# Kernel optimization log

Hardware: AMD Instinct MI355X
Metric: run time of the kernel (lower is better)

The kernel has to match this reference:

```python
import jax, jax.numpy as jnp
import numpy as np

B, N, S, K = 8, 4096, 1024, 16
C_IN, C_OUT = 128, 256
BN_EPS = 1e-5


def setup_inputs() -> dict:
    key = jax.random.key(0)
    ks = jax.random.split(key, 20)
    sc = 0.02
    p = {
        'xyz': jax.random.normal(ks[0], (B, N, 3), jnp.float32),
        'points': jax.random.normal(ks[1], (B, N, C_IN), jnp.float32),
        'wq': jax.random.normal(ks[2], (C_IN, C_OUT), jnp.float32) * sc,
        'wk': jax.random.normal(ks[3], (C_IN, C_OUT), jnp.float32) * sc,
        'wv': jax.random.normal(ks[4], (C_IN, C_OUT), jnp.float32) * sc,
        'dw1': jax.random.normal(ks[5], (3, C_OUT), jnp.float32) * sc,
        'db1': jnp.zeros((C_OUT,), jnp.float32),
        'dw2': jax.random.normal(ks[6], (C_OUT, C_OUT), jnp.float32) * sc,
        'db2': jnp.zeros((C_OUT,), jnp.float32),
        'gw1': jax.random.normal(ks[7], (C_OUT, C_OUT), jnp.float32) * sc,
        'gb1': jnp.zeros((C_OUT,), jnp.float32),
        'gw2': jax.random.normal(ks[8], (C_OUT, C_OUT), jnp.float32) * sc,
        'gb2': jnp.zeros((C_OUT,), jnp.float32),
        'lw': jax.random.normal(ks[9], (C_OUT, C_OUT), jnp.float32) * sc,
        'lb': jnp.zeros((C_OUT,), jnp.float32),
        'bn_g': jnp.ones((C_OUT,), jnp.float32),
        'bn_b': jnp.zeros((C_OUT,), jnp.float32),
    }
    return p


def _fps(xyz, npoint):
    # xyz: [N,3] -> farthest point sample indices [npoint] (deterministic start at 0,
    # matching torch impl with fixed seed semantics)
    n = xyz.shape[0]
    def step(carry, _):
        dist, far = carry
        centroid = xyz[far]                      # [3]
        d = jnp.sum((xyz - centroid) ** 2, -1)   # [N]
        dist = jnp.minimum(dist, d)
        return (dist, jnp.argmax(dist).astype(jnp.int32)), far
    init = (jnp.full((n,), 1e10, xyz.dtype), jnp.int32(0))
    _, idx = jax.lax.scan(step, init, None, length=npoint)
    return idx  # [npoint]


def _mlp2(x, w1, b1, w2, b2):
    return jax.nn.relu(x @ w1 + b1) @ w2 + b2


def reference(xyz, points, wq, wk, wv, dw1, db1, dw2, db2,
              gw1, gb1, gw2, gb2, lw, lb, bn_g, bn_b):
    # --- sample_and_group (FPS + KNN, knn=True) ---
    fps_idx = jax.vmap(lambda x: _fps(x, S))(xyz)                 # [B,S]
    new_xyz = jnp.take_along_axis(xyz, fps_idx[..., None], 1)     # [B,S,3]
    # squared distances sampled->all: [B,S,N]
    d2 = (jnp.sum(new_xyz**2, -1)[:, :, None]
          - 2.0 * jnp.einsum('bsc,bnc->bsn', new_xyz, xyz)
          + jnp.sum(xyz**2, -1)[:, None, :])
    knn_idx = jax.lax.top_k(-d2, K)[1]                            # [B,S,K]
    gather = jax.vmap(lambda a, i: a[i])
    knn_xyz = gather(xyz, knn_idx)                                # [B,S,K,3]
    knn_xyz_norm = knn_xyz - new_xyz[:, :, None]                  # centered coords
    knn_points = gather(points, knn_idx)                          # [B,S,K,C_in]
    sampled_points = jnp.take_along_axis(points, fps_idx[..., None], 1)  # [B,S,C_in]

    # --- vector attention ---
    q = sampled_points @ wq                                       # [B,S,C_out]
    k = knn_points @ wk                                           # [B,S,K,C_out]
    v = knn_points @ wv                                           # [B,S,K,C_out]
    pos_enc = _mlp2(knn_xyz_norm, dw1, db1, dw2, db2)             # [B,S,K,C_out]
    att = _mlp2(q[:, :, None] - k + pos_enc, gw1, gb1, gw2, gb2)  # [B,S,K,C_out]
    att = jax.nn.softmax(att / np.sqrt(C_OUT).astype(np.float32), axis=-2)
    res = jnp.einsum('bmnf,bmnf->bmf', att, v + pos_enc)          # [B,S,C_out]

    # --- fc_last + BatchNorm1d (training-mode batch stats, biased var) + ReLU ---
    res = res @ lw + lb
    mean = jnp.mean(res, axis=(0, 1))
    var = jnp.var(res, axis=(0, 1))
    res = bn_g * (res - mean) * jax.lax.rsqrt(var + BN_EPS) + bn_b
    res = jax.nn.relu(res)
    return new_xyz, res
```

## Files before the change

### kernel.cpp

```cpp
#include <hip/hip_runtime.h>

typedef unsigned long long ull;
typedef __attribute__((ext_vector_type(8))) short bf16x8;
typedef __attribute__((ext_vector_type(4))) float f32x4;

__device__ __forceinline__ unsigned short bf16b(float x){
    unsigned u = __float_as_uint(x);
    unsigned r = (u + 0x7FFFu + ((u >> 16) & 1u)) >> 16;
    return (unsigned short)r;
}
__device__ __forceinline__ float b2f(unsigned short u){
    return __uint_as_float(((unsigned)u) << 16);
}
__device__ __forceinline__ void st4(unsigned short* p, f32x4 v){
    ull pk = (ull)bf16b(v[0]) | (((ull)bf16b(v[1])) << 16)
           | (((ull)bf16b(v[2])) << 32) | (((ull)bf16b(v[3])) << 48);
    *(ull*)p = pk;
}
__device__ __forceinline__ f32x4 ld4(const unsigned short* p){
    ull pk = *(const ull*)p;
    f32x4 v;
    v[0] = b2f((unsigned short)pk);
    v[1] = b2f((unsigned short)(pk >> 16));
    v[2] = b2f((unsigned short)(pk >> 32));
    v[3] = b2f((unsigned short)(pk >> 48));
    return v;
}

#define DPPMAX(k, ctrl) do { \
    unsigned _lo = (unsigned)(k), _hi = (unsigned)((k) >> 32); \
    unsigned _l2 = (unsigned)__builtin_amdgcn_update_dpp((int)_lo, (int)_lo, (ctrl), 0xF, 0xF, false); \
    unsigned _h2 = (unsigned)__builtin_amdgcn_update_dpp((int)_hi, (int)_hi, (ctrl), 0xF, 0xF, false); \
    ull _k2 = (((ull)_h2) << 32) | _l2; \
    if (_k2 > (k)) (k) = _k2; \
} while (0)
#define DPPMIN(k, ctrl) do { \
    unsigned _lo = (unsigned)(k), _hi = (unsigned)((k) >> 32); \
    unsigned _l2 = (unsigned)__builtin_amdgcn_update_dpp((int)_lo, (int)_lo, (ctrl), 0xF, 0xF, false); \
    unsigned _h2 = (unsigned)__builtin_amdgcn_update_dpp((int)_hi, (int)_hi, (ctrl), 0xF, 0xF, false); \
    ull _k2 = (((ull)_h2) << 32) | _l2; \
    if (_k2 < (k)) (k) = _k2; \
} while (0)

template<int KT>
__device__ __forceinline__ int swz(int r, int c){
    return r * (KT * 32) + ((((c >> 3) + r) & (KT * 4 - 1)) << 3) + (c & 7);
}

template<int KT>
__device__ __forceinline__ void gemmT(const unsigned short* __restrict__ Wt,
                                      const unsigned short* __restrict__ Blds,
                                      int ch0, int lane, f32x4 acc[4][4])
{
    int i = lane & 15, q = lane >> 4;
#pragma unroll
    for (int kt = 0; kt < KT; kt++){
        int k0 = kt * 32 + q * 8;
        bf16x8 bfr[4], afr[4];
#pragma unroll
        for (int nt = 0; nt < 4; nt++)
            bfr[nt] = *(const bf16x8*)(Blds + swz<KT>(nt * 16 + i, k0));
#pragma unroll
        for (int mt = 0; mt < 4; mt++)
            afr[mt] = *(const bf16x8*)(Wt + (size_t)(ch0 + mt * 16 + i) * (KT * 32) + k0);
#pragma unroll
        for (int mt = 0; mt < 4; mt++)
#pragma unroll
            for (int nt = 0; nt < 4; nt++)
                acc[mt][nt] = __builtin_amdgcn_mfma_f32_16x16x32_bf16(afr[mt], bfr[nt], acc[mt][nt], 0, 0, 0);
    }
}

#define ZERO44(A) do { _Pragma("unroll") for (int _m = 0; _m < 4; _m++) \
    { _Pragma("unroll") for (int _n = 0; _n < 4; _n++) { A[_m][_n][0]=0.f;A[_m][_n][1]=0.f;A[_m][_n][2]=0.f;A[_m][_n][3]=0.f; } } } while(0)

__global__ __launch_bounds__(512, 2) void fps_mega(
    const float* __restrict__ xyz, float* __restrict__ nxyz_out, int* __restrict__ fps_idx,
    const float* __restrict__ pts, unsigned short* __restrict__ pts16,
    const float* __restrict__ wq, const float* __restrict__ wk, const float* __restrict__ wv,
    const float* __restrict__ dw2, const float* __restrict__ gw1, const float* __restrict__ gw2,
    const float* __restrict__ lw,
    float* __restrict__ wqT, unsigned short* __restrict__ wkT, unsigned short* __restrict__ wvT,
    unsigned short* __restrict__ dw2T, unsigned short* __restrict__ gw1T,
    unsigned short* __restrict__ gw2T, unsigned short* __restrict__ lwT,
    float* __restrict__ stats)
{
    __shared__ float sx[4096], sy[4096], sz[4096];
    __shared__ int farS[1024];
    __shared__ ull slotK[2][8];

    int blk = blockIdx.x;
    int t = threadIdx.x;

    if (blk >= 8){
        int aux = blk - 8;
        if (aux < 704){
            if (aux == 0) stats[t] = 0.f;
            int i = aux * 512 + t;
            if (i < 32768){ int n = i >> 7, k = i & 127; wqT[i] = wq[k * 256 + n]; return; } i -= 32768;
            if (i < 32768){ int n = i >> 7, k = i & 127; wkT[i] = bf16b(wk[k * 256 + n]); return; } i -= 32768;
            if (i < 32768){ int n = i >> 7, k = i & 127; wvT[i] = bf16b(wv[k * 256 + n]); return; } i -= 32768;
            if (i < 65536){ int n = i >> 8, k = i & 255; dw2T[i] = bf16b(dw2[k * 256 + n]); return; } i -= 65536;
            if (i < 65536){ int n = i >> 8, k = i & 255; gw1T[i] = bf16b(gw1[k * 256 + n]); return; } i -= 65536;
            if (i < 65536){ int n = i >> 8, k = i & 255; gw2T[i] = bf16b(gw2[k * 256 + n]); return; } i -= 65536;
            if (i < 65536){ int n = i >> 8, k = i & 255; lwT[i]  = bf16b(lw[k * 256 + n]); return; }
            return;
        }
        int i = ((aux - 704) * 512 + t) * 4;
        f32x4 v = *(const f32x4*)(pts + i);
        ull pk = (ull)bf16b(v[0]) | (((ull)bf16b(v[1])) << 16)
               | (((ull)bf16b(v[2])) << 32) | (((ull)bf16b(v[3])) << 48);
        *(ull*)(pts16 + i) = pk;
        return;
    }

    int b = blk;
    int lane = t & 63, wvi = t >> 6;
    for (int p = t; p < 4096; p += 512){
        const float* s = xyz + ((size_t)b * 4096 + p) * 3;
        sx[p] = s[0]; sy[p] = s[1]; sz[p] = s[2];
    }
    __syncthreads();
    float px[8], py[8], pz[8], dist[8];
    unsigned nplo[8];
#pragma unroll
    for (int j = 0; j < 8; j++){
        int p = t + (j << 9);
        px[j] = sx[p]; py[j] = sy[p]; pz[j] = sz[p];
        dist[j] = 1e10f;
        nplo[j] = ~(unsigned)p;
        asm volatile("" : "+v"(px[j]), "+v"(py[j]), "+v"(pz[j]), "+v"(nplo[j]));
    }
    int far = 0;
    float cx = sx[0], cy = sy[0], cz = sz[0];
    int par = 0;
    for (int s = 0; s < 1024; s++){
        if (t == 0) farS[s] = far;
        ull lb = 0;
#pragma unroll
        for (int j = 0; j < 8; j++){
            float dx = __fsub_rn(px[j], cx);
            float dy = __fsub_rn(py[j], cy);
            float dz = __fsub_rn(pz[j], cz);
            float d = __fadd_rn(__fadd_rn(__fmul_rn(dx, dx), __fmul_rn(dy, dy)), __fmul_rn(dz, dz));
            float nd = fminf(dist[j], d);
            dist[j] = nd;
            ull k2 = (((ull)__float_as_uint(nd)) << 32) | nplo[j];
            if (k2 > lb) lb = k2;
        }
        DPPMAX(lb, 0xB1); DPPMAX(lb, 0x4E); DPPMAX(lb, 0x141);
        DPPMAX(lb, 0x140); DPPMAX(lb, 0x142); DPPMAX(lb, 0x143);
        if (lane == 63) slotK[par][wvi] = lb;
        __syncthreads();
        ull k = slotK[par][lane & 7];
        DPPMAX(k, 0xB1); DPPMAX(k, 0x4E); DPPMAX(k, 0x141);
        far = (int)(~(unsigned)k);
        cx = sx[far]; cy = sy[far]; cz = sz[far];
        par ^= 1;
    }
    float* outp = nxyz_out + (size_t)b * 3072;
    for (int s2 = t; s2 < 1024; s2 += 512){
        int f = farS[s2];
        fps_idx[b * 1024 + s2] = f;
        outp[s2 * 3 + 0] = sx[f];
        outp[s2 * 3 + 1] = sy[f];
        outp[s2 * 3 + 2] = sz[f];
    }
}

__global__ __launch_bounds__(256) void knn_kernel(const float* __restrict__ xyz,
                                                  const float* __restrict__ nxyz,
                                                  int* __restrict__ knn_idx)
{
    __shared__ float d2s[4096];
    __shared__ ull kslot[4];
    int G = blockIdx.x; int b = G >> 10;
    int t = threadIdx.x, lane = t & 63, wvi = t >> 6;
    float qx = nxyz[(size_t)G * 3], qy = nxyz[(size_t)G * 3 + 1], qz = nxyz[(size_t)G * 3 + 2];
    float qq = qx * qx + qy * qy + qz * qz;
    for (int j = 0; j < 16; j++){
        int p = t + (j << 8);
        const float* s = xyz + ((size_t)b * 4096 + p) * 3;
        float x = s[0], y = s[1], z = s[2];
        d2s[p] = qq - 2.f * (qx * x + qy * y + qz * z) + (x * x + y * y + z * z);
    }
    __syncthreads();
    for (int r = 0; r < 16; r++){
        ull best = ~0ull;
#pragma unroll
        for (int j = 0; j < 16; j++){
            int p = t + (j << 8);
            unsigned bb = __float_as_uint(d2s[p]);
            bb = (bb & 0x80000000u) ? ~bb : (bb | 0x80000000u);
            ull key = (((ull)bb) << 32) | (unsigned)p;
            if (key < best) best = key;
        }
        DPPMIN(best, 0xB1); DPPMIN(best, 0x4E); DPPMIN(best, 0x141);
        DPPMIN(best, 0x140); DPPMIN(best, 0x142); DPPMIN(best, 0x143);
        if (lane == 63) kslot[wvi] = best;
        __syncthreads();
        if (t == 0){
            ull bk = kslot[0];
            for (int w = 1; w < 4; w++) if (kslot[w] < bk) bk = kslot[w];
            int p = (int)(unsigned)bk;
            knn_idx[(size_t)G * 16 + r] = p;
            d2s[p] = 3.0e38f;
        }
        __syncthreads();
    }
}

__global__ __launch_bounds__(256) void q_kernel(const float* __restrict__ points,
                                                const float* __restrict__ wqT,
                                                const int* __restrict__ fps_idx,
                                                float* __restrict__ qbuf)
{
    __shared__ float sp[8][128];
    int t = threadIdx.x;
    int g0 = blockIdx.x * 8;
    {
        int r = t >> 5, c = (t & 31) * 4;
        int G = g0 + r; int b = G >> 10; int p = fps_idx[G];
        const f32x4 v = *(const f32x4*)(points + ((size_t)b * 4096 + p) * 128 + c);
        *(f32x4*)&sp[r][c] = v;
    }
    __syncthreads();
    float acc[8] = {0.f,0.f,0.f,0.f,0.f,0.f,0.f,0.f};
    const float* wr = wqT + t * 128;
    for (int k = 0; k < 128; k += 4){
        f32x4 w = *(const f32x4*)(wr + k);
#pragma unroll
        for (int r = 0; r < 8; r++)
            acc[r] += w[0]*sp[r][k] + w[1]*sp[r][k+1] + w[2]*sp[r][k+2] + w[3]*sp[r][k+3];
    }
#pragma unroll
    for (int r = 0; r < 8; r++) qbuf[(size_t)(g0 + r) * 256 + t] = acc[r];
}

__global__ __launch_bounds__(256, 2) void fused_attn(
    const unsigned short* __restrict__ pts16,
    const float* __restrict__ xyz, const float* __restrict__ nxyz,
    const int* __restrict__ knn_idx, const float* __restrict__ qbuf,
    const unsigned short* __restrict__ wkT, const unsigned short* __restrict__ wvT,
    const unsigned short* __restrict__ dw2T, const unsigned short* __restrict__ gw1T,
    const unsigned short* __restrict__ gw2T,
    const float* __restrict__ dw1, const float* __restrict__ db1,
    const float* __restrict__ db2, const float* __restrict__ gb1, const float* __restrict__ gb2,
    unsigned short* __restrict__ resY)
{
    __shared__ unsigned short bufA[16384];
    __shared__ unsigned short bufU[16384];
    int t = threadIdx.x, lane = t & 63, wave = t >> 6;
    int i = lane & 15, q = lane >> 4;
    int G0 = blockIdx.x * 4;
    int ch0 = wave * 64;
    unsigned short* ptsA = bufU;
    float* dw1s  = (float*)(bufU + 8192);
    float* db1s  = (float*)(bufU + 9728);
    float* xyznS = (float*)(bufU + 10240);
    int*   idxs  = (int*)  (bufU + 10624);

    if (t < 64) idxs[t] = knn_idx[G0 * 16 + t];
    dw1s[t] = dw1[t]; dw1s[256 + t] = dw1[256 + t]; dw1s[512 + t] = dw1[512 + t];
    db1s[t] = db1[t];
    __syncthreads();

    if (t < 64){
        int G = G0 + (t >> 4); int bb = G >> 10; int p = idxs[t];
        const float* xp = xyz + ((size_t)bb * 4096 + p) * 3;
        const float* nz = nxyz + (size_t)G * 3;
        xyznS[t * 3 + 0] = xp[0] - nz[0];
        xyznS[t * 3 + 1] = xp[1] - nz[1];
        xyznS[t * 3 + 2] = xp[2] - nz[2];
    }
    {
        int r = t >> 2, seg = t & 3;
        int G = G0 + (r >> 4); int bb = G >> 10; int p = idxs[r];
        const uint4* src = (const uint4*)(pts16 + ((size_t)bb * 4096 + p) * 128 + seg * 32);
#pragma unroll
        for (int j = 0; j < 4; j++){
            uint4 v = src[j];
            *(uint4*)(ptsA + swz<4>(r, seg * 32 + j * 8)) = v;
        }
    }
    __syncthreads();

    {
        int r = lane;
        int o0 = wave * 64;
        float x = xyznS[r * 3], y = xyznS[r * 3 + 1], z = xyznS[r * 3 + 2];
#pragma unroll
        for (int j = 0; j < 64; j += 4){
            int o = o0 + j;
            f32x4 v;
#pragma unroll
            for (int e = 0; e < 4; e++)
                v[e] = fmaxf(db1s[o + e] + x * dw1s[o + e] + y * dw1s[256 + o + e] + z * dw1s[512 + o + e], 0.f);
            st4(bufA + swz<8>(r, o), v);
        }
    }
    __syncthreads();

    f32x4 accP[4][4]; ZERO44(accP);
    gemmT<8>(dw2T, bufA, ch0, lane, accP);
#pragma unroll
    for (int mt = 0; mt < 4; mt++){
        f32x4 d2v = *(const f32x4*)(db2 + ch0 + mt * 16 + q * 4);
#pragma unroll
        for (int nt = 0; nt < 4; nt++) accP[mt][nt] += d2v;
    }
    f32x4 accK[4][4]; ZERO44(accK);
    gemmT<4>(wkT, ptsA, ch0, lane, accK);
    __syncthreads();

#pragma unroll
    for (int mt = 0; mt < 4; mt++){
        int c = ch0 + mt * 16 + q * 4;
#pragma unroll
        for (int nt = 0; nt < 4; nt++){
            int r = nt * 16 + i;
            f32x4 qv = *(const f32x4*)(qbuf + (size_t)(G0 + nt) * 256 + c);
            f32x4 tv = qv - accK[mt][nt] + accP[mt][nt];
            st4(bufA + swz<8>(r, c), tv);
        }
    }
    f32x4 accV[4][4]; ZERO44(accV);
    gemmT<4>(wvT, ptsA, ch0, lane, accV);
    __syncthreads();

#pragma unroll
    for (int mt = 0; mt < 4; mt++){
        int c = ch0 + mt * 16 + q * 4;
#pragma unroll
        for (int nt = 0; nt < 4; nt++){
            int r = nt * 16 + i;
            f32x4 uv = accV[mt][nt] + accP[mt][nt];
            st4(bufU + swz<8>(r, c), uv);
        }
    }
    f32x4 acc1[4][4]; ZERO44(acc1);
    gemmT<8>(gw1T, bufA, ch0, lane, acc1);
    __syncthreads();

#pragma unroll
    for (int mt = 0; mt < 4; mt++){
        int c = ch0 + mt * 16 + q * 4;
        f32x4 g1v = *(const f32x4*)(gb1 + c);
#pragma unroll
        for (int nt = 0; nt < 4; nt++){
            int r = nt * 16 + i;
            f32x4 av = acc1[mt][nt] + g1v;
#pragma unroll
            for (int e = 0; e < 4; e++) av[e] = fmaxf(av[e], 0.f);
            st4(bufA + swz<8>(r, c), av);
        }
    }
    __syncthreads();

    f32x4 acc2[4][4]; ZERO44(acc2);
    gemmT<8>(gw2T, bufA, ch0, lane, acc2);
    __syncthreads();

#pragma unroll
    for (int mt = 0; mt < 4; mt++){
        int c = ch0 + mt * 16 + q * 4;
        f32x4 g2v = *(const f32x4*)(gb2 + c);
#pragma unroll
        for (int nt = 0; nt < 4; nt++){
            int r = nt * 16 + i;
            f32x4 ev;
#pragma unroll
            for (int e = 0; e < 4; e++) ev[e] = __expf((acc2[mt][nt][e] + g2v[e]) * 0.0625f);
            st4(bufA + swz<8>(r, c), ev);
        }
    }
    __syncthreads();

    {
        int g = t >> 6, c4 = (t & 63) * 4;
        f32x4 num; num[0]=0.f;num[1]=0.f;num[2]=0.f;num[3]=0.f;
        f32x4 den = num;
#pragma unroll
        for (int rr = 0; rr < 16; rr++){
            int r = g * 16 + rr;
            f32x4 e4 = ld4(bufA + swz<8>(r, c4));
            f32x4 u4 = ld4(bufU + swz<8>(r, c4));
            num += e4 * u4;
            den += e4;
        }
        f32x4 rv = num / den;
        st4(resY + (size_t)(G0 + g) * 256 + c4, rv);
    }
}

__global__ __launch_bounds__(256, 2) void z_gemm(const unsigned short* __restrict__ resY,
                                                 const unsigned short* __restrict__ lwT,
                                                 const float* __restrict__ lb,
                                                 float* __restrict__ zbuf,
                                                 float* __restrict__ stats)
{
    int t = threadIdx.x, lane = t & 63, wave = t >> 6;
    int i = lane & 15, q = lane >> 4;
    int row0 = blockIdx.x * 128;
    int ch0 = wave * 64;
    f32x4 acc[4][8];
#pragma unroll
    for (int mt = 0; mt < 4; mt++)
#pragma unroll
        for (int nt = 0; nt < 8; nt++){ acc[mt][nt][0]=0.f;acc[mt][nt][1]=0.f;acc[mt][nt][2]=0.f;acc[mt][nt][3]=0.f; }
#pragma unroll
    for (int kt = 0; kt < 8; kt++){
        int k0 = kt * 32 + q * 8;
        bf16x8 a[4], bb[8];
#pragma unroll
        for (int mt = 0; mt < 4; mt++)
            a[mt] = *(const bf16x8*)(lwT + (size_t)(ch0 + mt * 16 + i) * 256 + k0);
#pragma unroll
        for (int nt = 0; nt < 8; nt++)
            bb[nt] = *(const bf16x8*)(resY + (size_t)(row0 + nt * 16 + i) * 256 + k0);
#pragma unroll
        for (int mt = 0; mt < 4; mt++)
#pragma unroll
            for (int nt = 0; nt < 8; nt++)
                acc[mt][nt] = __builtin_amdgcn_mfma_f32_16x16x32_bf16(a[mt], bb[nt], acc[mt][nt], 0, 0, 0);
    }
    f32x4 s1[4], s2[4];
#pragma unroll
    for (int mt = 0; mt < 4; mt++){ s1[mt][0]=0.f;s1[mt][1]=0.f;s1[mt][2]=0.f;s1[mt][3]=0.f; s2[mt]=s1[mt]; }
#pragma unroll
    for (int mt = 0; mt < 4; mt++){
        int c = ch0 + mt * 16 + q * 4;
        f32x4 lb4 = *(const f32x4*)(lb + c);
#pragma unroll
        for (int nt = 0; nt < 8; nt++){
            int r = row0 + nt * 16 + i;
            f32x4 z = acc[mt][nt] + lb4;
            *(f32x4*)(zbuf + (size_t)r * 256 + c) = z;
            s1[mt] += z;
            s2[mt] += z * z;
        }
    }
    for (int m = 1; m < 16; m <<= 1){
#pragma unroll
        for (int mt = 0; mt < 4; mt++)
#pragma unroll
            for (int e = 0; e < 4; e++){
                s1[mt][e] += __shfl_xor(s1[mt][e], m);
                s2[mt][e] += __shfl_xor(s2[mt][e], m);
            }
    }
    if (i == 0){
#pragma unroll
        for (int mt = 0; mt < 4; mt++){
            int c = ch0 + mt * 16 + q * 4;
#pragma unroll
            for (int e = 0; e < 4; e++){
                atomicAdd(&stats[c + e], s1[mt][e]);
                atomicAdd(&stats[256 + c + e], s2[mt][e]);
            }
        }
    }
}

__global__ __launch_bounds__(256) void bn_kernel(const float* __restrict__ zbuf,
                                                 const float* __restrict__ stats,
                                                 const float* __restrict__ bn_g,
                                                 const float* __restrict__ bn_b,
                                                 float* __restrict__ out)
{
    int G = blockIdx.x, c = threadIdx.x;
    float mean = stats[c] * (1.f / 8192.f);
    float var = stats[256 + c] * (1.f / 8192.f) - mean * mean;
    float inv = rsqrtf(var + 1e-5f);
    float z = zbuf[(size_t)G * 256 + c];
    float y = bn_g[c] * (z - mean) * inv + bn_b[c];
    out[24576 + (size_t)G * 256 + c] = fmaxf(y, 0.f);
}

extern "C" void kernel_launch(void* const* d_in, const int* in_sizes, int n_in,
                              void* d_out, int out_size, void* d_ws, size_t ws_size,
                              hipStream_t stream)
{
    const float* xyz    = (const float*)d_in[0];
    const float* points = (const float*)d_in[1];
    const float* wq  = (const float*)d_in[2];
    const float* wk  = (const float*)d_in[3];
    const float* wv  = (const float*)d_in[4];
    const float* dw1 = (const float*)d_in[5];
    const float* db1 = (const float*)d_in[6];
    const float* dw2 = (const float*)d_in[7];
    const float* db2 = (const float*)d_in[8];
    const float* gw1 = (const float*)d_in[9];
    const float* gb1 = (const float*)d_in[10];
    const float* gw2 = (const float*)d_in[11];
    const float* gb2 = (const float*)d_in[12];
    const float* lw  = (const float*)d_in[13];
    const float* lb  = (const float*)d_in[14];
    const float* bn_g = (const float*)d_in[15];
    const float* bn_b = (const float*)d_in[16];
    float* out = (float*)d_out;

    char* ws = (char*)d_ws;
    int*            fps_idx = (int*)(ws + 0);
    int*            knn_idx = (int*)(ws + 32768);
    float*          qbuf    = (float*)(ws + 557056);
    unsigned short* pts16   = (unsigned short*)(ws + 8945664);
    unsigned short* wkT     = (unsigned short*)(ws + 17334272);
    unsigned short* wvT     = (unsigned short*)(ws + 17399808);
    unsigned short* dw2T    = (unsigned short*)(ws + 17465344);
    unsigned short* gw1T    = (unsigned short*)(ws + 17596416);
    unsigned short* gw2T    = (unsigned short*)(ws + 17727488);
    unsigned short* lwT     = (unsigned short*)(ws + 17858560);
    float*          wqT     = (float*)(ws + 17989632);
    unsigned short* resY    = (unsigned short*)(ws + 18120704);
    float*          zbuf    = (float*)(ws + 22315008);
    float*          stats   = (float*)(ws + 30703616);

    fps_mega<<<2760, 512, 0, stream>>>(xyz, out, fps_idx, points, pts16,
                                       wq, wk, wv, dw2, gw1, gw2, lw,
                                       wqT, wkT, wvT, dw2T, gw1T, gw2T, lwT, stats);
    knn_kernel<<<8192, 256, 0, stream>>>(xyz, out, knn_idx);
    q_kernel<<<1024, 256, 0, stream>>>(points, wqT, fps_idx, qbuf);
    fused_attn<<<2048, 256, 0, stream>>>(pts16, xyz, out, knn_idx, qbuf,
                                         wkT, wvT, dw2T, gw1T, gw2T,
                                         dw1, db1, db2, gb1, gb2, resY);
    z_gemm<<<64, 256, 0, stream>>>(resY, lwT, lb, zbuf, stats);
    bn_kernel<<<8192, 256, 0, stream>>>(zbuf, stats, bn_g, bn_b, out);
}
```

Measured before the change: 1.051 ms.

## Use packed FP32 math and split float-max/index reduction in FPS loop

The farthest-point-sampling inner loop now computes squared distances with packed v_pk_add/v_pk_mul on pairs of points. The per-wave argmax is split into two steps: a 32-bit float max reduction across the wave, then a second 32-bit DPP reduction over the indices whose distance equals that max. This replaces the 64-bit key reduction, which needed two DPP moves and a 64-bit compare per step. Index tie-breaking is kept by selecting the largest inverted index. Rounding differs slightly because the subtraction is done as an add of the negated centroid, though this should give the same result.

```diff
diff --git a/kernel.cpp b/kernel.cpp
--- a/kernel.cpp
+++ b/kernel.cpp
@@ -3,6 +3,7 @@
 typedef unsigned long long ull;
 typedef __attribute__((ext_vector_type(8))) short bf16x8;
 typedef __attribute__((ext_vector_type(4))) float f32x4;
+typedef __attribute__((ext_vector_type(2))) float f32x2;
 
 __device__ __forceinline__ unsigned short bf16b(float x){
     unsigned u = __float_as_uint(x);
@@ -25,6 +26,13 @@
     v[2] = b2f((unsigned short)(pk >> 32));
     v[3] = b2f((unsigned short)(pk >> 48));
     return v;
+}
+
+__device__ __forceinline__ f32x2 pk_add(f32x2 a, f32x2 b){
+    f32x2 r; asm("v_pk_add_f32 %0, %1, %2" : "=v"(r) : "v"(a), "v"(b)); return r;
+}
+__device__ __forceinline__ f32x2 pk_mul(f32x2 a, f32x2 b){
+    f32x2 r; asm("v_pk_mul_f32 %0, %1, %2" : "=v"(r) : "v"(a), "v"(b)); return r;
 }
 
 #define DPPMAX(k, ctrl) do { \
@@ -41,6 +49,15 @@
     ull _k2 = (((ull)_h2) << 32) | _l2; \
     if (_k2 < (k)) (k) = _k2; \
 } while (0)
+#define DPPMAXF(x, ctrl) do { \
+    float _o = __uint_as_float((unsigned)__builtin_amdgcn_update_dpp( \
+        (int)__float_as_uint(x), (int)__float_as_uint(x), (ctrl), 0xF, 0xF, false)); \
+    (x) = fmaxf((x), _o); \
+} while (0)
+#define DPPMAXU(x, ctrl) do { \
+    unsigned _o = (unsigned)__builtin_amdgcn_update_dpp((int)(x), (int)(x), (ctrl), 0xF, 0xF, false); \
+    (x) = (_o > (x)) ? _o : (x); \
+} while (0)
 
 template<int KT>
 __device__ __forceinline__ int swz(int r, int c){
@@ -121,36 +138,61 @@
         sx[p] = s[0]; sy[p] = s[1]; sz[p] = s[2];
     }
     __syncthreads();
-    float px[8], py[8], pz[8], dist[8];
+    f32x2 px2[4], py2[4], pz2[4];
+    float dist[8];
     unsigned nplo[8];
 #pragma unroll
-    for (int j = 0; j < 8; j++){
-        int p = t + (j << 9);
-        px[j] = sx[p]; py[j] = sy[p]; pz[j] = sz[p];
-        dist[j] = 1e10f;
-        nplo[j] = ~(unsigned)p;
-        asm volatile("" : "+v"(px[j]), "+v"(py[j]), "+v"(pz[j]), "+v"(nplo[j]));
+    for (int k = 0; k < 4; k++){
+        int p0 = t + (k << 10), p1 = p0 + 512;
+        px2[k][0] = sx[p0]; px2[k][1] = sx[p1];
+        py2[k][0] = sy[p0]; py2[k][1] = sy[p1];
+        pz2[k][0] = sz[p0]; pz2[k][1] = sz[p1];
+        dist[2*k] = 1e10f; dist[2*k+1] = 1e10f;
+        nplo[2*k] = ~(unsigned)p0; nplo[2*k+1] = ~(unsigned)p1;
+        asm volatile("" : "+v"(px2[k]), "+v"(py2[k]), "+v"(pz2[k]));
     }
     int far = 0;
     float cx = sx[0], cy = sy[0], cz = sz[0];
     int par = 0;
     for (int s = 0; s < 1024; s++){
         if (t == 0) farS[s] = far;
-        ull lb = 0;
-#pragma unroll
-        for (int j = 0; j < 8; j++){
-            float dx = __fsub_rn(px[j], cx);
-            float dy = __fsub_rn(py[j], cy);
-            float dz = __fsub_rn(pz[j], cz);
-            float d = __fadd_rn(__fadd_rn(__fmul_rn(dx, dx), __fmul_rn(dy, dy)), __fmul_rn(dz, dz));
-            float nd = fminf(dist[j], d);
-            dist[j] = nd;
-            ull k2 = (((ull)__float_as_uint(nd)) << 32) | nplo[j];
-            if (k2 > lb) lb = k2;
-        }
-        DPPMAX(lb, 0xB1); DPPMAX(lb, 0x4E); DPPMAX(lb, 0x141);
-        DPPMAX(lb, 0x140); DPPMAX(lb, 0x142); DPPMAX(lb, 0x143);
-        if (lane == 63) slotK[par][wvi] = lb;
+        f32x2 ncx, ncy, ncz;
+        ncx[0] = -cx; ncx[1] = -cx;
+        ncy[0] = -cy; ncy[1] = -cy;
+        ncz[0] = -cz; ncz[1] = -cz;
+        float bmax = 0.f;
+#pragma unroll
+        for (int k = 0; k < 4; k++){
+            f32x2 dx = pk_add(px2[k], ncx);
+            f32x2 dy = pk_add(py2[k], ncy);
+            f32x2 dz = pk_add(pz2[k], ncz);
+            f32x2 d2 = pk_add(pk_add(pk_mul(dx, dx), pk_mul(dy, dy)), pk_mul(dz, dz));
+            float n0 = fminf(dist[2*k],     d2[0]);
+            float n1 = fminf(dist[2*k + 1], d2[1]);
+            dist[2*k] = n0; dist[2*k+1] = n1;
+            bmax = fmaxf(bmax, fmaxf(n0, n1));
+        }
+        DPPMAXF(bmax, 0xB1); DPPMAXF(bmax, 0x4E); DPPMAXF(bmax, 0x141);
+        DPPMAXF(bmax, 0x140); DPPMAXF(bmax, 0x142); DPPMAXF(bmax, 0x143);
+        unsigned wmb = (unsigned)__builtin_amdgcn_readlane((int)__float_as_uint(bmax), 63);
+        unsigned c0 = (__float_as_uint(dist[0]) == wmb) ? nplo[0] : 0u;
+        unsigned c1 = (__float_as_uint(dist[1]) == wmb) ? nplo[1] : 0u;
+        unsigned c2 = (__float_as_uint(dist[2]) == wmb) ? nplo[2] : 0u;
+        unsigned c3 = (__float_as_uint(dist[3]) == wmb) ? nplo[3] : 0u;
+        unsigned c4 = (__float_as_uint(dist[4]) == wmb) ? nplo[4] : 0u;
+        unsigned c5 = (__float_as_uint(dist[5]) == wmb) ? nplo[5] : 0u;
+        unsigned c6 = (__float_as_uint(dist[6]) == wmb) ? nplo[6] : 0u;
+        unsigned c7 = (__float_as_uint(dist[7]) == wmb) ? nplo[7] : 0u;
+        unsigned m0 = c0 > c1 ? c0 : c1;
+        unsigned m1 = c2 > c3 ? c2 : c3;
+        unsigned m2 = c4 > c5 ? c4 : c5;
+        unsigned m3 = c6 > c7 ? c6 : c7;
+        m0 = m0 > m1 ? m0 : m1;
+        m2 = m2 > m3 ? m2 : m3;
+        unsigned cand = m0 > m2 ? m0 : m2;
+        DPPMAXU(cand, 0xB1); DPPMAXU(cand, 0x4E); DPPMAXU(cand, 0x141);
+        DPPMAXU(cand, 0x140); DPPMAXU(cand, 0x142); DPPMAXU(cand, 0x143);
+        if (lane == 63) slotK[par][wvi] = (((ull)wmb) << 32) | (ull)cand;
         __syncthreads();
         ull k = slotK[par][lane & 7];
         DPPMAX(k, 0xB1); DPPMAX(k, 0x4E); DPPMAX(k, 0x141);
```

New measurement: 1.111 ms. 5.6% more time.

## Fuse FPS, KNN, query and attention into persistent kernel overlapping FPS progress

Applied to the files above, without the earlier changes.

Replaces the separate FPS, KNN, q-projection and attention kernels with one persistent 256-block kernel. Eight blocks run FPS and publish progress every 16 samples through atomic counters. The other blocks first do the weight and points preprocessing, then spin-wait and process 8-centroid chunks (KNN, q, attention) as soon as their centroids are ready. This hides the serial FPS latency behind the downstream work, at the cost of spin-wait synchronisation and a reliance on all 256 blocks being co-resident. ctrl aliases the zbuf region, which is only written later by z_gemm.

```diff
diff --git a/kernel.cpp b/kernel.cpp
--- a/kernel.cpp
+++ b/kernel.cpp
@@ -74,112 +74,16 @@
 #define ZERO44(A) do { _Pragma("unroll") for (int _m = 0; _m < 4; _m++) \
     { _Pragma("unroll") for (int _n = 0; _n < 4; _n++) { A[_m][_n][0]=0.f;A[_m][_n][1]=0.f;A[_m][_n][2]=0.f;A[_m][_n][3]=0.f; } } } while(0)
 
-__global__ __launch_bounds__(512, 2) void fps_mega(
-    const float* __restrict__ xyz, float* __restrict__ nxyz_out, int* __restrict__ fps_idx,
-    const float* __restrict__ pts, unsigned short* __restrict__ pts16,
-    const float* __restrict__ wq, const float* __restrict__ wk, const float* __restrict__ wv,
-    const float* __restrict__ dw2, const float* __restrict__ gw1, const float* __restrict__ gw2,
-    const float* __restrict__ lw,
-    float* __restrict__ wqT, unsigned short* __restrict__ wkT, unsigned short* __restrict__ wvT,
-    unsigned short* __restrict__ dw2T, unsigned short* __restrict__ gw1T,
-    unsigned short* __restrict__ gw2T, unsigned short* __restrict__ lwT,
-    float* __restrict__ stats)
-{
-    __shared__ float sx[4096], sy[4096], sz[4096];
-    __shared__ int farS[1024];
-    __shared__ ull slotK[2][8];
-
-    int blk = blockIdx.x;
-    int t = threadIdx.x;
-
-    if (blk >= 8){
-        int aux = blk - 8;
-        if (aux < 704){
-            if (aux == 0) stats[t] = 0.f;
-            int i = aux * 512 + t;
-            if (i < 32768){ int n = i >> 7, k = i & 127; wqT[i] = wq[k * 256 + n]; return; } i -= 32768;
-            if (i < 32768){ int n = i >> 7, k = i & 127; wkT[i] = bf16b(wk[k * 256 + n]); return; } i -= 32768;
-            if (i < 32768){ int n = i >> 7, k = i & 127; wvT[i] = bf16b(wv[k * 256 + n]); return; } i -= 32768;
-            if (i < 65536){ int n = i >> 8, k = i & 255; dw2T[i] = bf16b(dw2[k * 256 + n]); return; } i -= 65536;
-            if (i < 65536){ int n = i >> 8, k = i & 255; gw1T[i] = bf16b(gw1[k * 256 + n]); return; } i -= 65536;
-            if (i < 65536){ int n = i >> 8, k = i & 255; gw2T[i] = bf16b(gw2[k * 256 + n]); return; } i -= 65536;
-            if (i < 65536){ int n = i >> 8, k = i & 255; lwT[i]  = bf16b(lw[k * 256 + n]); return; }
-            return;
-        }
-        int i = ((aux - 704) * 512 + t) * 4;
-        f32x4 v = *(const f32x4*)(pts + i);
-        ull pk = (ull)bf16b(v[0]) | (((ull)bf16b(v[1])) << 16)
-               | (((ull)bf16b(v[2])) << 32) | (((ull)bf16b(v[3])) << 48);
-        *(ull*)(pts16 + i) = pk;
-        return;
-    }
-
-    int b = blk;
-    int lane = t & 63, wvi = t >> 6;
-    for (int p = t; p < 4096; p += 512){
-        const float* s = xyz + ((size_t)b * 4096 + p) * 3;
-        sx[p] = s[0]; sy[p] = s[1]; sz[p] = s[2];
-    }
-    __syncthreads();
-    float px[8], py[8], pz[8], dist[8];
-    unsigned nplo[8];
-#pragma unroll
-    for (int j = 0; j < 8; j++){
-        int p = t + (j << 9);
-        px[j] = sx[p]; py[j] = sy[p]; pz[j] = sz[p];
-        dist[j] = 1e10f;
-        nplo[j] = ~(unsigned)p;
-        asm volatile("" : "+v"(px[j]), "+v"(py[j]), "+v"(pz[j]), "+v"(nplo[j]));
-    }
-    int far = 0;
-    float cx = sx[0], cy = sy[0], cz = sz[0];
-    int par = 0;
-    for (int s = 0; s < 1024; s++){
-        if (t == 0) farS[s] = far;
-        ull lb = 0;
-#pragma unroll
-        for (int j = 0; j < 8; j++){
-            float dx = __fsub_rn(px[j], cx);
-            float dy = __fsub_rn(py[j], cy);
-            float dz = __fsub_rn(pz[j], cz);
-            float d = __fadd_rn(__fadd_rn(__fmul_rn(dx, dx), __fmul_rn(dy, dy)), __fmul_rn(dz, dz));
-            float nd = fminf(dist[j], d);
-            dist[j] = nd;
-            ull k2 = (((ull)__float_as_uint(nd)) << 32) | nplo[j];
-            if (k2 > lb) lb = k2;
-        }
-        DPPMAX(lb, 0xB1); DPPMAX(lb, 0x4E); DPPMAX(lb, 0x141);
-        DPPMAX(lb, 0x140); DPPMAX(lb, 0x142); DPPMAX(lb, 0x143);
-        if (lane == 63) slotK[par][wvi] = lb;
-        __syncthreads();
-        ull k = slotK[par][lane & 7];
-        DPPMAX(k, 0xB1); DPPMAX(k, 0x4E); DPPMAX(k, 0x141);
-        far = (int)(~(unsigned)k);
-        cx = sx[far]; cy = sy[far]; cz = sz[far];
-        par ^= 1;
-    }
-    float* outp = nxyz_out + (size_t)b * 3072;
-    for (int s2 = t; s2 < 1024; s2 += 512){
-        int f = farS[s2];
-        fps_idx[b * 1024 + s2] = f;
-        outp[s2 * 3 + 0] = sx[f];
-        outp[s2 * 3 + 1] = sy[f];
-        outp[s2 * 3 + 2] = sz[f];
-    }
-}
-
-__global__ __launch_bounds__(256) void knn_kernel(const float* __restrict__ xyz,
-                                                  const float* __restrict__ nxyz,
-                                                  int* __restrict__ knn_idx)
-{
-    __shared__ float d2s[4096];
-    __shared__ ull kslot[4];
-    int G = blockIdx.x; int b = G >> 10;
-    int t = threadIdx.x, lane = t & 63, wvi = t >> 6;
+__device__ __forceinline__ void knn_one(int t2, int G,
+        const float* __restrict__ xyz, const float* __restrict__ nxyz,
+        int* __restrict__ knn_idx, float* d2s, ull* kslot)
+{
+    int b = G >> 10;
+    int lane = t2 & 63, wvi = t2 >> 6;
     float qx = nxyz[(size_t)G * 3], qy = nxyz[(size_t)G * 3 + 1], qz = nxyz[(size_t)G * 3 + 2];
     float qq = qx * qx + qy * qy + qz * qz;
     for (int j = 0; j < 16; j++){
-        int p = t + (j << 8);
+        int p = t2 + (j << 8);
         const float* s = xyz + ((size_t)b * 4096 + p) * 3;
         float x = s[0], y = s[1], z = s[2];
         d2s[p] = qq - 2.f * (qx * x + qy * y + qz * z) + (x * x + y * y + z * z);
@@ -189,7 +93,7 @@
         ull best = ~0ull;
 #pragma unroll
         for (int j = 0; j < 16; j++){
-            int p = t + (j << 8);
+            int p = t2 + (j << 8);
             unsigned bb = __float_as_uint(d2s[p]);
             bb = (bb & 0x80000000u) ? ~bb : (bb | 0x80000000u);
             ull key = (((ull)bb) << 32) | (unsigned)p;
@@ -199,7 +103,7 @@
         DPPMIN(best, 0x140); DPPMIN(best, 0x142); DPPMIN(best, 0x143);
         if (lane == 63) kslot[wvi] = best;
         __syncthreads();
-        if (t == 0){
+        if (t2 == 0){
             ull bk = kslot[0];
             for (int w = 1; w < 4; w++) if (kslot[w] < bk) bk = kslot[w];
             int p = (int)(unsigned)bk;
@@ -210,34 +114,7 @@
     }
 }
 
-__global__ __launch_bounds__(256) void q_kernel(const float* __restrict__ points,
-                                                const float* __restrict__ wqT,
-                                                const int* __restrict__ fps_idx,
-                                                float* __restrict__ qbuf)
-{
-    __shared__ float sp[8][128];
-    int t = threadIdx.x;
-    int g0 = blockIdx.x * 8;
-    {
-        int r = t >> 5, c = (t & 31) * 4;
-        int G = g0 + r; int b = G >> 10; int p = fps_idx[G];
-        const f32x4 v = *(const f32x4*)(points + ((size_t)b * 4096 + p) * 128 + c);
-        *(f32x4*)&sp[r][c] = v;
-    }
-    __syncthreads();
-    float acc[8] = {0.f,0.f,0.f,0.f,0.f,0.f,0.f,0.f};
-    const float* wr = wqT + t * 128;
-    for (int k = 0; k < 128; k += 4){
-        f32x4 w = *(const f32x4*)(wr + k);
-#pragma unroll
-        for (int r = 0; r < 8; r++)
-            acc[r] += w[0]*sp[r][k] + w[1]*sp[r][k+1] + w[2]*sp[r][k+2] + w[3]*sp[r][k+3];
-    }
-#pragma unroll
-    for (int r = 0; r < 8; r++) qbuf[(size_t)(g0 + r) * 256 + t] = acc[r];
-}
-
-__global__ __launch_bounds__(256, 2) void fused_attn(
+__device__ void attn_unit(int t, char* base, int G0,
     const unsigned short* __restrict__ pts16,
     const float* __restrict__ xyz, const float* __restrict__ nxyz,
     const int* __restrict__ knn_idx, const float* __restrict__ qbuf,
@@ -248,11 +125,10 @@
     const float* __restrict__ db2, const float* __restrict__ gb1, const float* __restrict__ gb2,
     unsigned short* __restrict__ resY)
 {
-    __shared__ unsigned short bufA[16384];
-    __shared__ unsigned short bufU[16384];
-    int t = threadIdx.x, lane = t & 63, wave = t >> 6;
+    unsigned short* bufA = (unsigned short*)base;
+    unsigned short* bufU = (unsigned short*)(base + 32768);
+    int lane = t & 63, wave = t >> 6;
     int i = lane & 15, q = lane >> 4;
-    int G0 = blockIdx.x * 4;
     int ch0 = wave * 64;
     unsigned short* ptsA = bufU;
     float* dw1s  = (float*)(bufU + 8192);
@@ -390,6 +266,187 @@
         }
         f32x4 rv = num / den;
         st4(resY + (size_t)(G0 + g) * 256 + c4, rv);
+    }
+}
+
+__device__ void do_chunk(int t, int c, char* SM,
+    const float* __restrict__ xyz, const float* __restrict__ nxyz,
+    const float* __restrict__ points, const float* __restrict__ wqT,
+    const int* __restrict__ fps_idx, int* __restrict__ knn_idx, float* __restrict__ qbuf,
+    const unsigned short* __restrict__ pts16,
+    const unsigned short* __restrict__ wkT, const unsigned short* __restrict__ wvT,
+    const unsigned short* __restrict__ dw2T, const unsigned short* __restrict__ gw1T,
+    const unsigned short* __restrict__ gw2T,
+    const float* __restrict__ dw1, const float* __restrict__ db1,
+    const float* __restrict__ db2, const float* __restrict__ gb1, const float* __restrict__ gb2,
+    unsigned short* __restrict__ resY)
+{
+    int g0 = c * 8;
+    int sub = t >> 8, t2 = t & 255;
+    float* d2s = (float*)(SM + sub * 16384);
+    ull* kslot = (ull*)(SM + 131072) + sub * 4;
+    for (int r4 = 0; r4 < 4; r4++)
+        knn_one(t2, g0 + r4 * 2 + sub, xyz, nxyz, knn_idx, d2s, kslot);
+    __syncthreads();
+    {
+        float* sp = (float*)SM;
+        if (t < 256){
+            int r = t >> 5, c4 = (t & 31) * 4;
+            int G = g0 + r; int b = G >> 10; int p = fps_idx[G];
+            *(f32x4*)(sp + r * 128 + c4) = *(const f32x4*)(points + ((size_t)b * 4096 + p) * 128 + c4);
+        }
+        __syncthreads();
+        float acc[4] = {0.f, 0.f, 0.f, 0.f};
+        const float* wr = wqT + t2 * 128;
+        for (int k = 0; k < 128; k += 4){
+            f32x4 w = *(const f32x4*)(wr + k);
+#pragma unroll
+            for (int r = 0; r < 4; r++){
+                const float* row = sp + (sub * 4 + r) * 128;
+                acc[r] += w[0]*row[k] + w[1]*row[k+1] + w[2]*row[k+2] + w[3]*row[k+3];
+            }
+        }
+#pragma unroll
+        for (int r = 0; r < 4; r++) qbuf[(size_t)(g0 + sub * 4 + r) * 256 + t2] = acc[r];
+        __syncthreads();
+    }
+    attn_unit(t2, SM + sub * 65536, g0 + sub * 4, pts16, xyz, nxyz, knn_idx, qbuf,
+              wkT, wvT, dw2T, gw1T, gw2T, dw1, db1, db2, gb1, gb2, resY);
+    __syncthreads();
+}
+
+__global__ void init_ctrl(int* __restrict__ ctrl)
+{
+    if (threadIdx.x < 16) ctrl[threadIdx.x] = 0;
+}
+
+__global__ __launch_bounds__(512, 2) void mega(
+    const float* __restrict__ xyz, float* __restrict__ nxyz_out, int* __restrict__ fps_idx,
+    const float* __restrict__ pts, unsigned short* __restrict__ pts16,
+    const float* __restrict__ wq, const float* __restrict__ wk, const float* __restrict__ wv,
+    const float* __restrict__ dw2, const float* __restrict__ gw1, const float* __restrict__ gw2,
+    const float* __restrict__ lw,
+    float* __restrict__ wqT, unsigned short* __restrict__ wkT, unsigned short* __restrict__ wvT,
+    unsigned short* __restrict__ dw2T, unsigned short* __restrict__ gw1T,
+    unsigned short* __restrict__ gw2T, unsigned short* __restrict__ lwT,
+    float* __restrict__ stats,
+    const float* __restrict__ dw1, const float* __restrict__ db1, const float* __restrict__ db2,
+    const float* __restrict__ gb1, const float* __restrict__ gb2,
+    int* __restrict__ knn_idx, float* __restrict__ qbuf, unsigned short* __restrict__ resY,
+    int* __restrict__ ctrl)
+{
+    __shared__ __align__(16) char SM[132096];
+    int blk = blockIdx.x, t = threadIdx.x;
+
+    if (blk < 8){
+        int b = blk;
+        int lane = t & 63, wvi = t >> 6;
+        float* sx = (float*)SM;
+        float* sy = (float*)(SM + 16384);
+        float* sz = (float*)(SM + 32768);
+        int* farS = (int*)(SM + 49152);
+        ull (*slotK)[8] = (ull(*)[8])(SM + 53248);
+        for (int p = t; p < 4096; p += 512){
+            const float* s = xyz + ((size_t)b * 4096 + p) * 3;
+            sx[p] = s[0]; sy[p] = s[1]; sz[p] = s[2];
+        }
+        __syncthreads();
+        float px[8], py[8], pz[8], dist[8];
+        unsigned nplo[8];
+#pragma unroll
+        for (int j = 0; j < 8; j++){
+            int p = t + (j << 9);
+            px[j] = sx[p]; py[j] = sy[p]; pz[j] = sz[p];
+            dist[j] = 1e10f;
+            nplo[j] = ~(unsigned)p;
+            asm volatile("" : "+v"(px[j]), "+v"(py[j]), "+v"(pz[j]), "+v"(nplo[j]));
+        }
+        int far = 0;
+        float cx = sx[0], cy = sy[0], cz = sz[0];
+        int par = 0;
+        for (int s = 0; s < 1024; s++){
+            if (t == 0) farS[s] = far;
+            ull lb = 0;
+#pragma unroll
+            for (int j = 0; j < 8; j++){
+                float dx = __fsub_rn(px[j], cx);
+                float dy = __fsub_rn(py[j], cy);
+                float dz = __fsub_rn(pz[j], cz);
+                float d = __fadd_rn(__fadd_rn(__fmul_rn(dx, dx), __fmul_rn(dy, dy)), __fmul_rn(dz, dz));
+                float nd = fminf(dist[j], d);
+                dist[j] = nd;
+                ull k2 = (((ull)__float_as_uint(nd)) << 32) | nplo[j];
+                if (k2 > lb) lb = k2;
+            }
+            DPPMAX(lb, 0xB1); DPPMAX(lb, 0x4E); DPPMAX(lb, 0x141);
+            DPPMAX(lb, 0x140); DPPMAX(lb, 0x142); DPPMAX(lb, 0x143);
+            if (lane == 63) slotK[par][wvi] = lb;
+            __syncthreads();
+            ull k = slotK[par][lane & 7];
+            DPPMAX(k, 0xB1); DPPMAX(k, 0x4E); DPPMAX(k, 0x141);
+            far = (int)(~(unsigned)k);
+            cx = sx[far]; cy = sy[far]; cz = sz[far];
+            if (((s & 15) == 15) && wvi == 7){
+                int s0 = s - 15;
+                if (lane < 16){
+                    fps_idx[b * 1024 + s0 + lane] = farS[s0 + lane];
+                } else {
+                    int idx = lane - 16;
+                    int st = s0 + idx / 3, d = idx - (idx / 3) * 3;
+                    int f = farS[st];
+                    float v = (d == 0) ? sx[f] : ((d == 1) ? sy[f] : sz[f]);
+                    nxyz_out[(size_t)b * 3072 + st * 3 + d] = v;
+                }
+                __threadfence();
+                if (lane == 0) atomicExch(&ctrl[b], s + 1);
+            }
+            par ^= 1;
+        }
+        if (t == 0){ while (atomicAdd(&ctrl[8], 0) < 248) __builtin_amdgcn_s_sleep(16); }
+        __syncthreads();
+        __threadfence();
+        do_chunk(t, b * 128 + 127, SM, xyz, nxyz_out, pts, wqT, fps_idx, knn_idx, qbuf,
+                 pts16, wkT, wvT, dw2T, gw1T, gw2T, dw1, db1, db2, gb1, gb2, resY);
+        return;
+    }
+
+    int w = blk - 8;
+    for (int base = w; base < 704; base += 248){
+        if (base == 0) stats[t & 511] = 0.f;
+        int i = base * 512 + t;
+        if (i < 32768){ int n = i >> 7, kk = i & 127; wqT[i] = wq[kk * 256 + n]; }
+        else if (i < 65536){ int j = i - 32768; int n = j >> 7, kk = j & 127; wkT[j] = bf16b(wk[kk * 256 + n]); }
+        else if (i < 98304){ int j = i - 65536; int n = j >> 7, kk = j & 127; wvT[j] = bf16b(wv[kk * 256 + n]); }
+        else if (i < 163840){ int j = i - 98304; int n = j >> 8, kk = j & 255; dw2T[j] = bf16b(dw2[kk * 256 + n]); }
+        else if (i < 229376){ int j = i - 163840; int n = j >> 8, kk = j & 255; gw1T[j] = bf16b(gw1[kk * 256 + n]); }
+        else if (i < 294912){ int j = i - 229376; int n = j >> 8, kk = j & 255; gw2T[j] = bf16b(gw2[kk * 256 + n]); }
+        else { int j = i - 294912; int n = j >> 8, kk = j & 255; lwT[j] = bf16b(lw[kk * 256 + n]); }
+    }
+    for (int base = w; base < 2048; base += 248){
+        int i = (base * 512 + t) * 4;
+        f32x4 v = *(const f32x4*)(pts + i);
+        ull pk = (ull)bf16b(v[0]) | (((ull)bf16b(v[1])) << 16)
+               | (((ull)bf16b(v[2])) << 32) | (((ull)bf16b(v[3])) << 48);
+        *(ull*)(pts16 + i) = pk;
+    }
+    __threadfence();
+    __syncthreads();
+    if (t == 0){
+        atomicAdd(&ctrl[8], 1);
+        while (atomicAdd(&ctrl[8], 0) < 248) __builtin_amdgcn_s_sleep(16);
+    }
+    __syncthreads();
+    __threadfence();
+    for (int j = 0; j < 5; j++){
+        int p = w + 248 * j;
+        if (p >= 1016) break;
+        int bb = p & 7, cc = p >> 3;
+        int need = cc * 8 + 8;
+        if (t == 0){ while (atomicAdd(&ctrl[bb], 0) < need) __builtin_amdgcn_s_sleep(64); }
+        __syncthreads();
+        __threadfence();
+        do_chunk(t, bb * 128 + cc, SM, xyz, nxyz_out, pts, wqT, fps_idx, knn_idx, qbuf,
+                 pts16, wkT, wvT, dw2T, gw1T, gw2T, dw1, db1, db2, gb1, gb2, resY);
     }
 }
 
@@ -515,15 +572,14 @@
     unsigned short* resY    = (unsigned short*)(ws + 18120704);
     float*          zbuf    = (float*)(ws + 22315008);
     float*          stats   = (float*)(ws + 30703616);
-
-    fps_mega<<<2760, 512, 0, stream>>>(xyz, out, fps_idx, points, pts16,
-                                       wq, wk, wv, dw2, gw1, gw2, lw,
-                                       wqT, wkT, wvT, dw2T, gw1T, gw2T, lwT, stats);
-    knn_kernel<<<8192, 256, 0, stream>>>(xyz, out, knn_idx);
-    q_kernel<<<1024, 256, 0, stream>>>(points, wqT, fps_idx, qbuf);
-    fused_attn<<<2048, 256, 0, stream>>>(pts16, xyz, out, knn_idx, qbuf,
-                                         wkT, wvT, dw2T, gw1T, gw2T,
-                                         dw1, db1, db2, gb1, gb2, resY);
+    int*            ctrl    = (int*)(ws + 22315008);
+
+    init_ctrl<<<1, 64, 0, stream>>>(ctrl);
+    mega<<<256, 512, 0, stream>>>(xyz, out, fps_idx, points, pts16,
+                                  wq, wk, wv, dw2, gw1, gw2, lw,
+                                  wqT, wkT, wvT, dw2T, gw1T, gw2T, lwT, stats,
+                                  dw1, db1, db2, gb1, gb2,
+                                  knn_idx, qbuf, resY, ctrl);
     z_gemm<<<64, 256, 0, stream>>>(resY, lwT, lb, zbuf, stats);
     bn_kernel<<<8192, 256, 0, stream>>>(zbuf, stats, bn_g, bn_b, out);
 }
```

Result: faster. 971.7 us (-7.6%).

## Fuse KNN, query projection and attention into one chunked kernel

Applied to the files above, without the earlier changes.

Merges the separate knn, q-projection and fused attention kernels into a single 512-thread kernel. Each block handles 8 sampled points, and its two 256-thread halves share a 132KB LDS arena. This removes two launches and the inter-kernel dependency gaps. In exchange it uses very large LDS per block (one block per CU at most) and __syncthreads across both halves. Those barriers sit inside the KNN loop and attn_unit, which may serialize work and reduce occupancy compared with the prior 2-blocks-per-CU attention kernel.

```diff
diff --git a/kernel.cpp b/kernel.cpp
--- a/kernel.cpp
+++ b/kernel.cpp
@@ -168,18 +168,15 @@
     }
 }
 
-__global__ __launch_bounds__(256) void knn_kernel(const float* __restrict__ xyz,
-                                                  const float* __restrict__ nxyz,
-                                                  int* __restrict__ knn_idx)
-{
-    __shared__ float d2s[4096];
-    __shared__ ull kslot[4];
-    int G = blockIdx.x; int b = G >> 10;
-    int t = threadIdx.x, lane = t & 63, wvi = t >> 6;
-    float qx = nxyz[(size_t)G * 3], qy = nxyz[(size_t)G * 3 + 1], qz = nxyz[(size_t)G * 3 + 2];
+__device__ __forceinline__ void knn_one(int t2, int G, float qx, float qy, float qz,
+        const float* __restrict__ xyz,
+        int* __restrict__ knn_idx, float* d2s, ull* kslot)
+{
+    int b = G >> 10;
+    int lane = t2 & 63, wvi = t2 >> 6;
     float qq = qx * qx + qy * qy + qz * qz;
     for (int j = 0; j < 16; j++){
-        int p = t + (j << 8);
+        int p = t2 + (j << 8);
         const float* s = xyz + ((size_t)b * 4096 + p) * 3;
         float x = s[0], y = s[1], z = s[2];
         d2s[p] = qq - 2.f * (qx * x + qy * y + qz * z) + (x * x + y * y + z * z);
@@ -189,7 +186,7 @@
         ull best = ~0ull;
 #pragma unroll
         for (int j = 0; j < 16; j++){
-            int p = t + (j << 8);
+            int p = t2 + (j << 8);
             unsigned bb = __float_as_uint(d2s[p]);
             bb = (bb & 0x80000000u) ? ~bb : (bb | 0x80000000u);
             ull key = (((ull)bb) << 32) | (unsigned)p;
@@ -199,7 +196,7 @@
         DPPMIN(best, 0x140); DPPMIN(best, 0x142); DPPMIN(best, 0x143);
         if (lane == 63) kslot[wvi] = best;
         __syncthreads();
-        if (t == 0){
+        if (t2 == 0){
             ull bk = kslot[0];
             for (int w = 1; w < 4; w++) if (kslot[w] < bk) bk = kslot[w];
             int p = (int)(unsigned)bk;
@@ -210,36 +207,9 @@
     }
 }
 
-__global__ __launch_bounds__(256) void q_kernel(const float* __restrict__ points,
-                                                const float* __restrict__ wqT,
-                                                const int* __restrict__ fps_idx,
-                                                float* __restrict__ qbuf)
-{
-    __shared__ float sp[8][128];
-    int t = threadIdx.x;
-    int g0 = blockIdx.x * 8;
-    {
-        int r = t >> 5, c = (t & 31) * 4;
-        int G = g0 + r; int b = G >> 10; int p = fps_idx[G];
-        const f32x4 v = *(const f32x4*)(points + ((size_t)b * 4096 + p) * 128 + c);
-        *(f32x4*)&sp[r][c] = v;
-    }
-    __syncthreads();
-    float acc[8] = {0.f,0.f,0.f,0.f,0.f,0.f,0.f,0.f};
-    const float* wr = wqT + t * 128;
-    for (int k = 0; k < 128; k += 4){
-        f32x4 w = *(const f32x4*)(wr + k);
-#pragma unroll
-        for (int r = 0; r < 8; r++)
-            acc[r] += w[0]*sp[r][k] + w[1]*sp[r][k+1] + w[2]*sp[r][k+2] + w[3]*sp[r][k+3];
-    }
-#pragma unroll
-    for (int r = 0; r < 8; r++) qbuf[(size_t)(g0 + r) * 256 + t] = acc[r];
-}
-
-__global__ __launch_bounds__(256, 2) void fused_attn(
+__device__ void attn_unit(int t, char* base, int G0, const float* nxL4,
     const unsigned short* __restrict__ pts16,
-    const float* __restrict__ xyz, const float* __restrict__ nxyz,
+    const float* __restrict__ xyz,
     const int* __restrict__ knn_idx, const float* __restrict__ qbuf,
     const unsigned short* __restrict__ wkT, const unsigned short* __restrict__ wvT,
     const unsigned short* __restrict__ dw2T, const unsigned short* __restrict__ gw1T,
@@ -248,11 +218,10 @@
     const float* __restrict__ db2, const float* __restrict__ gb1, const float* __restrict__ gb2,
     unsigned short* __restrict__ resY)
 {
-    __shared__ unsigned short bufA[16384];
-    __shared__ unsigned short bufU[16384];
-    int t = threadIdx.x, lane = t & 63, wave = t >> 6;
+    unsigned short* bufA = (unsigned short*)base;
+    unsigned short* bufU = (unsigned short*)(base + 32768);
+    int lane = t & 63, wave = t >> 6;
     int i = lane & 15, q = lane >> 4;
-    int G0 = blockIdx.x * 4;
     int ch0 = wave * 64;
     unsigned short* ptsA = bufU;
     float* dw1s  = (float*)(bufU + 8192);
@@ -268,7 +237,7 @@
     if (t < 64){
         int G = G0 + (t >> 4); int bb = G >> 10; int p = idxs[t];
         const float* xp = xyz + ((size_t)bb * 4096 + p) * 3;
-        const float* nz = nxyz + (size_t)G * 3;
+        const float* nz = nxL4 + (t >> 4) * 3;
         xyznS[t * 3 + 0] = xp[0] - nz[0];
         xyznS[t * 3 + 1] = xp[1] - nz[1];
         xyznS[t * 3 + 2] = xp[2] - nz[2];
@@ -391,6 +360,68 @@
         f32x4 rv = num / den;
         st4(resY + (size_t)(G0 + g) * 256 + c4, rv);
     }
+}
+
+__global__ __launch_bounds__(512) void chunk_kernel(
+    const float* __restrict__ xyz, const float* __restrict__ nxyz,
+    const float* __restrict__ points, const float* __restrict__ wqT,
+    const int* __restrict__ fps_idx, int* __restrict__ knn_idx, float* __restrict__ qbuf,
+    const unsigned short* __restrict__ pts16,
+    const unsigned short* __restrict__ wkT, const unsigned short* __restrict__ wvT,
+    const unsigned short* __restrict__ dw2T, const unsigned short* __restrict__ gw1T,
+    const unsigned short* __restrict__ gw2T,
+    const float* __restrict__ dw1, const float* __restrict__ db1,
+    const float* __restrict__ db2, const float* __restrict__ gb1, const float* __restrict__ gb2,
+    unsigned short* __restrict__ resY)
+{
+    __shared__ __align__(16) char SM[132096];
+    int t = threadIdx.x;
+    int c = blockIdx.x;
+    int g0 = c * 8;
+    int sub = t >> 8, t2 = t & 255;
+    int*   fpsL = (int*)  (SM + 131200);
+    float* nxL  = (float*)(SM + 131232);
+
+    if (t < 32){
+        if (t < 8) fpsL[t] = fps_idx[g0 + t];
+        else ((int*)nxL)[t - 8] = ((const int*)nxyz)[(size_t)g0 * 3 + (t - 8)];
+    }
+    __syncthreads();
+
+    float* d2s = (float*)(SM + sub * 16384);
+    ull* kslot = (ull*)(SM + 131072) + sub * 4;
+    for (int r4 = 0; r4 < 4; r4++){
+        int gl = r4 * 2 + sub;
+        knn_one(t2, g0 + gl, nxL[gl * 3], nxL[gl * 3 + 1], nxL[gl * 3 + 2],
+                xyz, knn_idx, d2s, kslot);
+    }
+    __syncthreads();
+
+    {
+        float* sp = (float*)SM;
+        if (t < 256){
+            int r = t >> 5, c4 = (t & 31) * 4;
+            int G = g0 + r; int b = G >> 10; int p = fpsL[r];
+            *(f32x4*)(sp + r * 128 + c4) = *(const f32x4*)(points + ((size_t)b * 4096 + p) * 128 + c4);
+        }
+        __syncthreads();
+        float acc[4] = {0.f, 0.f, 0.f, 0.f};
+        const float* wr = wqT + t2 * 128;
+        for (int k = 0; k < 128; k += 4){
+            f32x4 w = *(const f32x4*)(wr + k);
+#pragma unroll
+            for (int r = 0; r < 4; r++){
+                const float* row = sp + (sub * 4 + r) * 128;
+                acc[r] += w[0]*row[k] + w[1]*row[k+1] + w[2]*row[k+2] + w[3]*row[k+3];
+            }
+        }
+#pragma unroll
+        for (int r = 0; r < 4; r++) qbuf[(size_t)(g0 + sub * 4 + r) * 256 + t2] = acc[r];
+        __syncthreads();
+    }
+
+    attn_unit(t2, SM + sub * 65536, g0 + sub * 4, nxL + sub * 12, pts16, xyz, knn_idx, qbuf,
+              wkT, wvT, dw2T, gw1T, gw2T, dw1, db1, db2, gb1, gb2, resY);
 }
 
 __global__ __launch_bounds__(256, 2) void z_gemm(const unsigned short* __restrict__ resY,
@@ -519,11 +550,9 @@
     fps_mega<<<2760, 512, 0, stream>>>(xyz, out, fps_idx, points, pts16,
                                        wq, wk, wv, dw2, gw1, gw2, lw,
                                        wqT, wkT, wvT, dw2T, gw1T, gw2T, lwT, stats);
-    knn_kernel<<<8192, 256, 0, stream>>>(xyz, out, knn_idx);
-    q_kernel<<<1024, 256, 0, stream>>>(points, wqT, fps_idx, qbuf);
-    fused_attn<<<2048, 256, 0, stream>>>(pts16, xyz, out, knn_idx, qbuf,
-                                         wkT, wvT, dw2T, gw1T, gw2T,
-                                         dw1, db1, db2, gb1, gb2, resY);
+    chunk_kernel<<<1024, 512, 0, stream>>>(xyz, out, points, wqT, fps_idx, knn_idx, qbuf,
+                                           pts16, wkT, wvT, dw2T, gw1T, gw2T,
+                                           dw1, db1, db2, gb1, gb2, resY);
     z_gemm<<<64, 256, 0, stream>>>(resY, lwT, lb, zbuf, stats);
     bn_kernel<<<8192, 256, 0, stream>>>(zbuf, stats, bn_g, bn_b, out);
 }
```

Result: slower. 1.183 ms (+12.5%).
